# Kernel tuning notes

Hardware: AMD Instinct MI355X
Metric: run time of the kernel (lower is better)

## Reference

```python
import jax, jax.numpy as jnp
import numpy as np

B, LTEXT, LVIS, D, H = 16, 128, 4096, 1024, 16
HD = D // H


def setup_inputs() -> dict:
    key = jax.random.key(0)
    ks = jax.random.split(key, 8)
    s = 0.02
    return {
        'hidden_states': jax.random.normal(ks[0], (B, LVIS, D), jnp.float32),
        'text_states': jax.random.normal(ks[1], (LTEXT, B, D), jnp.float32),
        'Wq': jax.random.normal(ks[2], (D, D), jnp.float32) * s,
        'bq': jnp.zeros((D,), jnp.float32),
        'Wk': jax.random.normal(ks[3], (D, D), jnp.float32) * s,
        'bk': jnp.zeros((D,), jnp.float32),
        'Wv': jax.random.normal(ks[4], (D, D), jnp.float32) * s,
        'bv': jnp.zeros((D,), jnp.float32),
        'Wo': jax.random.normal(ks[5], (D, D), jnp.float32) * s,
        'bo': jnp.zeros((D,), jnp.float32),
    }


def reference(hidden_states, text_states, Wq, bq, Wk, bk, Wv, bv, Wo, bo):
    # text_states: (L_text, B, D) -- code unpacks text_len, bsz from dims 0,1
    # hidden_states: (B, L_vis, D) -- key/value source
    Ltext, bsz, d = text_states.shape
    Lvis = hidden_states.shape[1]
    scale = HD ** -0.5

    # projections (torch Linear x @ W.T + b, here W stored already transposed)
    q = (text_states @ Wq + bq) * scale
    # faithful to torch .view: flatten memory then reshape to (B, Ltext, H, hd)
    q = q.reshape(bsz, Ltext, H, HD).transpose(0, 2, 1, 3)        # (B,H,Lt,hd)
    k = (hidden_states @ Wk + bk).reshape(bsz, Lvis, H, HD).transpose(0, 2, 1, 3)
    v = (hidden_states @ Wv + bv).reshape(bsz, Lvis, H, HD).transpose(0, 2, 1, 3)

    attn = jax.nn.softmax(jnp.einsum('bhtd,bhsd->bhts', q, k), axis=-1)  # (B,H,Lt,Lv)
    text_guided_vision = jnp.einsum('bhts,bhsd->bhtd', attn, v)          # (B,H,Lt,hd)
    # second matmul with transposed attention weights: P^T @ (P V)
    out = jnp.einsum('bhts,bhtd->bhsd', attn, text_guided_vision)        # (B,H,Lv,hd)

    out = out.transpose(0, 2, 1, 3).reshape(bsz, Lvis, d)
    return out @ Wo + bo
```

## Files before the change

### kernel.cpp

```cpp
#include <hip/hip_runtime.h>
#include <stdint.h>

typedef short  s16x8 __attribute__((ext_vector_type(8)));
typedef float  f32x4 __attribute__((ext_vector_type(4)));

__device__ __forceinline__ unsigned short f2bf(float f) {
  unsigned u = __builtin_bit_cast(unsigned, f);
  u = (u + 0x7fffu + ((u >> 16) & 1u)) >> 16;
  return (unsigned short)u;
}

__device__ __forceinline__ void glds16(const void* g, void* l) {
  __builtin_amdgcn_global_load_lds((const __attribute__((address_space(1))) void*)g,
                                   (__attribute__((address_space(3))) void*)l, 16, 0, 0);
}

__device__ __forceinline__ f32x4 mfma16(s16x8 a, s16x8 b, f32x4 c) {
  return __builtin_amdgcn_mfma_f32_16x16x32_bf16(a, b, c, 0, 0, 0);
}

__global__ __launch_bounds__(256) void kt_cvt(const float* __restrict__ X,
                                              unsigned short* __restrict__ Y) {
  const size_t N8 = (size_t)16 * 4096 * 1024 / 8;
  for (size_t i = (size_t)blockIdx.x * 256 + threadIdx.x; i < N8;
       i += (size_t)gridDim.x * 256) {
    const float* g = X + i * 8;
    f32x4 a = *(const f32x4*)g;
    f32x4 b = *(const f32x4*)(g + 4);
    s16x8 o;
    o[0]=f2bf(a[0]); o[1]=f2bf(a[1]); o[2]=f2bf(a[2]); o[3]=f2bf(a[3]);
    o[4]=f2bf(b[0]); o[5]=f2bf(b[1]); o[6]=f2bf(b[2]); o[7]=f2bf(b[3]);
    *(s16x8*)(Y + i * 8) = o;
  }
}

__global__ void kt_transpose(const float* __restrict__ W, unsigned short* __restrict__ WT) {
  __shared__ float tile[64][65];
  int n0 = blockIdx.x * 64, k0 = blockIdx.y * 64;
  int tx = threadIdx.x, ty = threadIdx.y;
  #pragma unroll
  for (int r = ty; r < 64; r += 4)
    tile[r][tx] = W[(size_t)(k0 + r) * 1024 + n0 + tx];
  __syncthreads();
  #pragma unroll
  for (int r = ty; r < 64; r += 4)
    WT[(size_t)(n0 + r) * 1024 + k0 + tx] = f2bf(tile[tx][r]);
}

template <int MODE>
__global__ __launch_bounds__(256, 2) void kt_gemm(
    const void* __restrict__ Ain, const unsigned short* __restrict__ BT,
    const float* __restrict__ bias, void* __restrict__ Cout) {
  __shared__ __align__(16) unsigned short As[128 * 32];
  __shared__ __align__(16) unsigned short Bs[128 * 32];
  const int tid = threadIdx.x, lane = tid & 63, wave = tid >> 6;
  const int l15 = lane & 15, quad = lane >> 4;
  const int wr = wave >> 1, wc = wave & 1;
  const int n0 = blockIdx.x * 128, m0 = blockIdx.y * 128;

  f32x4 acc[4][4] = {};
  for (int k0 = 0; k0 < 1024; k0 += 32) {
    __syncthreads();
    #pragma unroll
    for (int i = 0; i < 2; ++i) {
      int rowb = (wave * 2 + i) * 16 + (lane >> 2);
      glds16(BT + (size_t)(n0 + rowb) * 1024 + k0 + (lane & 3) * 8,
             &Bs[(wave * 2 + i) * 512]);
    }
    if constexpr (MODE == 1) {
      const unsigned short* A = (const unsigned short*)Ain;
      #pragma unroll
      for (int i = 0; i < 2; ++i) {
        int rowa = (wave * 2 + i) * 16 + (lane >> 2);
        glds16(A + (size_t)(m0 + rowa) * 1024 + k0 + (lane & 3) * 8,
               &As[(wave * 2 + i) * 512]);
      }
    } else {
      const float* A = (const float*)Ain;
      int row = tid >> 1, ks = (tid & 1) * 16;
      const float* g = &A[(size_t)(m0 + row) * 1024 + k0 + ks];
      f32x4 fa = *(const f32x4*)(g);
      f32x4 fb = *(const f32x4*)(g + 4);
      f32x4 fc = *(const f32x4*)(g + 8);
      f32x4 fd = *(const f32x4*)(g + 12);
      s16x8 lo, hi;
      lo[0]=f2bf(fa[0]); lo[1]=f2bf(fa[1]); lo[2]=f2bf(fa[2]); lo[3]=f2bf(fa[3]);
      lo[4]=f2bf(fb[0]); lo[5]=f2bf(fb[1]); lo[6]=f2bf(fb[2]); lo[7]=f2bf(fb[3]);
      hi[0]=f2bf(fc[0]); hi[1]=f2bf(fc[1]); hi[2]=f2bf(fc[2]); hi[3]=f2bf(fc[3]);
      hi[4]=f2bf(fd[0]); hi[5]=f2bf(fd[1]); hi[6]=f2bf(fd[2]); hi[7]=f2bf(fd[3]);
      *(s16x8*)&As[row * 32 + ks] = lo;
      *(s16x8*)&As[row * 32 + ks + 8] = hi;
    }
    __syncthreads();
    s16x8 a[4], b[4];
    #pragma unroll
    for (int i = 0; i < 4; ++i) a[i] = *(const s16x8*)&As[(wr * 64 + i * 16 + l15) * 32 + quad * 8];
    #pragma unroll
    for (int j = 0; j < 4; ++j) b[j] = *(const s16x8*)&Bs[(wc * 64 + j * 16 + l15) * 32 + quad * 8];
    #pragma unroll
    for (int i = 0; i < 4; ++i)
      #pragma unroll
      for (int j = 0; j < 4; ++j) acc[i][j] = mfma16(a[i], b[j], acc[i][j]);
  }
  #pragma unroll
  for (int j = 0; j < 4; ++j) {
    int col = n0 + wc * 64 + j * 16 + l15;
    float bv = bias[col];
    #pragma unroll
    for (int i = 0; i < 4; ++i)
      #pragma unroll
      for (int r = 0; r < 4; ++r) {
        int row = m0 + wr * 64 + i * 16 + quad * 4 + r;
        float v = acc[i][j][r] + bv;
        if constexpr (MODE == 0) {
          v *= 0.125f;
          size_t idx = ((size_t)((row >> 7) * 16 + (col >> 6)) * 128 + (row & 127)) * 64 + (col & 63);
          ((unsigned short*)Cout)[idx] = f2bf(v);
        } else {
          ((float*)Cout)[(size_t)row * 1024 + col] = v;
        }
      }
  }
}

__global__ __launch_bounds__(256, 2) void kt_gemm_kv(
    const unsigned short* __restrict__ A, const unsigned short* __restrict__ BTk,
    const unsigned short* __restrict__ BTv, const float* __restrict__ biask,
    const float* __restrict__ biasv, unsigned short* __restrict__ Ko,
    unsigned short* __restrict__ Vo) {
  __shared__ __align__(16) unsigned short As[128 * 32];
  __shared__ __align__(16) unsigned short BsK[128 * 32];
  __shared__ __align__(16) unsigned short BsV[128 * 32];
  const int tid = threadIdx.x, lane = tid & 63, wave = tid >> 6;
  const int l15 = lane & 15, quad = lane >> 4;
  const int wr = wave >> 1, wc = wave & 1;
  const int n0 = blockIdx.x * 128, m0 = blockIdx.y * 128;
  f32x4 accK[4][4] = {}, accV[4][4] = {};
  for (int k0 = 0; k0 < 1024; k0 += 32) {
    __syncthreads();
    #pragma unroll
    for (int i = 0; i < 2; ++i) {
      int rowt = (wave * 2 + i) * 16 + (lane >> 2);
      int colo = (lane & 3) * 8;
      size_t goffb = (size_t)(n0 + rowt) * 1024 + k0 + colo;
      glds16(BTk + goffb, &BsK[(wave * 2 + i) * 512]);
      glds16(BTv + goffb, &BsV[(wave * 2 + i) * 512]);
      glds16(A + (size_t)(m0 + rowt) * 1024 + k0 + colo, &As[(wave * 2 + i) * 512]);
    }
    __syncthreads();
    s16x8 a[4], bk_[4], bv_[4];
    #pragma unroll
    for (int i = 0; i < 4; ++i) a[i] = *(const s16x8*)&As[(wr * 64 + i * 16 + l15) * 32 + quad * 8];
    #pragma unroll
    for (int j = 0; j < 4; ++j) bk_[j] = *(const s16x8*)&BsK[(wc * 64 + j * 16 + l15) * 32 + quad * 8];
    #pragma unroll
    for (int j = 0; j < 4; ++j) bv_[j] = *(const s16x8*)&BsV[(wc * 64 + j * 16 + l15) * 32 + quad * 8];
    #pragma unroll
    for (int i = 0; i < 4; ++i)
      #pragma unroll
      for (int j = 0; j < 4; ++j) {
        accK[i][j] = mfma16(a[i], bk_[j], accK[i][j]);
        accV[i][j] = mfma16(a[i], bv_[j], accV[i][j]);
      }
  }
  #pragma unroll
  for (int j = 0; j < 4; ++j) {
    int col = n0 + wc * 64 + j * 16 + l15;
    float bkv = biask[col], bvv = biasv[col];
    int hcol = col >> 6, dcol = col & 63;
    #pragma unroll
    for (int i = 0; i < 4; ++i)
      #pragma unroll
      for (int r = 0; r < 4; ++r) {
        int row = m0 + wr * 64 + i * 16 + quad * 4 + r;
        int bb = row >> 12, s = row & 4095;
        Ko[(((size_t)bb * 16 + hcol) * 4096 + s) * 64 + dcol] = f2bf(accK[i][j][r] + bkv);
        Vo[(((size_t)bb * 16 + hcol) * 64 + dcol) * 4096 + s] = f2bf(accV[i][j][r] + bvv);
      }
  }
}

__global__ __launch_bounds__(256, 2) void kt_attn1(
    const unsigned short* __restrict__ Qb, const unsigned short* __restrict__ Kb,
    const unsigned short* __restrict__ Vt, float* __restrict__ RpT,
    float* __restrict__ Zp) {
  __shared__ __align__(16) unsigned short Ks[128 * 64];
  __shared__ __align__(16) unsigned short Vts[64 * 128];
  __shared__ __align__(16) unsigned short Es[128 * 128];
  const int tid = threadIdx.x, lane = tid & 63, wave = tid >> 6;
  const int l15 = lane & 15, quad = lane >> 4;
  const int qidx = blockIdx.x, h = blockIdx.y, b = blockIdx.z;
  const int bh = b * 16 + h;
  const size_t kbase = (size_t)bh * 4096 * 64;
  const size_t vbase = (size_t)bh * 64 * 4096;
  s16x8 qa[2][2];
  #pragma unroll
  for (int i = 0; i < 2; ++i)
    #pragma unroll
    for (int kk = 0; kk < 2; ++kk)
      qa[i][kk] = *(const s16x8*)&Qb[((size_t)bh * 128 + wave * 32 + i * 16 + l15) * 64 + kk * 32 + quad * 8];
  s16x8 bones;
  { unsigned short o = (l15 == 0) ? (unsigned short)0x3F80 : (unsigned short)0;
    #pragma unroll
    for (int c2 = 0; c2 < 8; ++c2) bones[c2] = (short)o; }
  f32x4 Racc[2][4] = {};
  f32x4 Zacc[2] = {};
  for (int ch = 0; ch < 8; ++ch) {
    const int s0 = qidx * 1024 + ch * 128;
    __syncthreads();
    #pragma unroll
    for (int i = 0; i < 4; ++i) {
      int srow = (wave * 4 + i) * 8 + (lane >> 3);
      glds16(Kb + kbase + (size_t)(s0 + srow) * 64 + (lane & 7) * 8, &Ks[(wave * 4 + i) * 512]);
    }
    #pragma unroll
    for (int i = 0; i < 4; ++i) {
      int drow = (wave * 4 + i) * 4 + (lane >> 4);
      glds16(Vt + vbase + (size_t)drow * 4096 + s0 + (lane & 15) * 8, &Vts[(wave * 4 + i) * 512]);
    }
    __syncthreads();
    f32x4 Sacc[2][8] = {};
    #pragma unroll
    for (int kk = 0; kk < 2; ++kk) {
      s16x8 bk_[8];
      #pragma unroll
      for (int j = 0; j < 8; ++j)
        bk_[j] = *(const s16x8*)&Ks[(j * 16 + l15) * 64 + kk * 32 + quad * 8];
      #pragma unroll
      for (int i = 0; i < 2; ++i)
        #pragma unroll
        for (int j = 0; j < 8; ++j) Sacc[i][j] = mfma16(qa[i][kk], bk_[j], Sacc[i][j]);
    }
    #pragma unroll
    for (int i = 0; i < 2; ++i)
      #pragma unroll
      for (int j = 0; j < 8; ++j)
        #pragma unroll
        for (int r = 0; r < 4; ++r)
          Es[(wave * 32 + i * 16 + quad * 4 + r) * 128 + j * 16 + l15] = f2bf(__expf(Sacc[i][j][r]));
    #pragma unroll
    for (int kk = 0; kk < 4; ++kk) {
      s16x8 ea[2];
      #pragma unroll
      for (int i2 = 0; i2 < 2; ++i2)
        ea[i2] = *(const s16x8*)&Es[(wave * 32 + i2 * 16 + l15) * 128 + kk * 32 + quad * 8];
      s16x8 bv_[4];
      #pragma unroll
      for (int jd = 0; jd < 4; ++jd)
        bv_[jd] = *(const s16x8*)&Vts[(jd * 16 + l15) * 128 + kk * 32 + quad * 8];
      #pragma unroll
      for (int i2 = 0; i2 < 2; ++i2) {
        #pragma unroll
        for (int jd = 0; jd < 4; ++jd) Racc[i2][jd] = mfma16(ea[i2], bv_[jd], Racc[i2][jd]);
        Zacc[i2] = mfma16(ea[i2], bones, Zacc[i2]);
      }
    }
  }
  #pragma unroll
  for (int i2 = 0; i2 < 2; ++i2) {
    int t0 = wave * 32 + i2 * 16 + quad * 4;
    #pragma unroll
    for (int jd = 0; jd < 4; ++jd) {
      int d = jd * 16 + l15;
      *(f32x4*)&RpT[(((size_t)qidx * 256 + bh) * 64 + d) * 128 + t0] = Racc[i2][jd];
    }
    if (l15 == 0) {
      #pragma unroll
      for (int r = 0; r < 4; ++r)
        Zp[((size_t)qidx * 256 + bh) * 128 + t0 + r] = Zacc[i2][r];
    }
  }
}

__global__ void kt_reduce(const float* __restrict__ RpT, const float* __restrict__ Zp,
                          unsigned short* __restrict__ Gt) {
  size_t id = (size_t)blockIdx.x * 256 + threadIdx.x;
  int t = (int)(id & 127);
  size_t bh = id >> 13;
  float z = 0.f, r = 0.f;
  #pragma unroll
  for (int q = 0; q < 4; ++q) {
    z += Zp[(size_t)q * 32768 + bh * 128 + t];
    r += RpT[(size_t)q * 2097152 + id];
  }
  Gt[id] = f2bf(r / (z * z));
}

__global__ __launch_bounds__(256, 2) void kt_attn2(
    const unsigned short* __restrict__ Qb, const unsigned short* __restrict__ Kb,
    const unsigned short* __restrict__ Gt, unsigned short* __restrict__ Ao) {
  __shared__ __align__(16) unsigned short Ks[64 * 64];
  __shared__ __align__(16) unsigned short EsT[64 * 136];
  const int tid = threadIdx.x, lane = tid & 63, wave = tid >> 6;
  const int l15 = lane & 15, quad = lane >> 4;
  const int c = blockIdx.x, h = blockIdx.y, b = blockIdx.z;
  const int bh = b * 16 + h;
  s16x8 qf[8][2], gf[4][4];
  #pragma unroll
  for (int jt = 0; jt < 8; ++jt)
    #pragma unroll
    for (int kk = 0; kk < 2; ++kk)
      qf[jt][kk] = *(const s16x8*)&Qb[((size_t)bh * 128 + jt * 16 + l15) * 64 + kk * 32 + quad * 8];
  #pragma unroll
  for (int jd = 0; jd < 4; ++jd)
    #pragma unroll
    for (int kk = 0; kk < 4; ++kk)
      gf[jd][kk] = *(const s16x8*)&Gt[((size_t)bh * 64 + jd * 16 + l15) * 128 + kk * 32 + quad * 8];
  const size_t kbase = (size_t)bh * 4096 * 64;
  for (int it = 0; it < 16; ++it) {
    const int s0 = c * 1024 + it * 64;
    __syncthreads();
    #pragma unroll
    for (int i = 0; i < 2; ++i) {
      int srow = (wave * 2 + i) * 8 + (lane >> 3);
      glds16(Kb + kbase + (size_t)(s0 + srow) * 64 + (lane & 7) * 8, &Ks[(wave * 2 + i) * 512]);
    }
    __syncthreads();
    f32x4 Sacc[8] = {};
    #pragma unroll
    for (int kk = 0; kk < 2; ++kk) {
      s16x8 a = *(const s16x8*)&Ks[(wave * 16 + l15) * 64 + kk * 32 + quad * 8];
      #pragma unroll
      for (int jt = 0; jt < 8; ++jt) Sacc[jt] = mfma16(a, qf[jt][kk], Sacc[jt]);
    }
    #pragma unroll
    for (int jt = 0; jt < 8; ++jt)
      #pragma unroll
      for (int r = 0; r < 4; ++r)
        EsT[(wave * 16 + quad * 4 + r) * 136 + jt * 16 + l15] = f2bf(__expf(Sacc[jt][r]));
    f32x4 Oacc[4] = {};
    #pragma unroll
    for (int kk = 0; kk < 4; ++kk) {
      s16x8 ea = *(const s16x8*)&EsT[(wave * 16 + l15) * 136 + kk * 32 + quad * 8];
      #pragma unroll
      for (int jd = 0; jd < 4; ++jd) Oacc[jd] = mfma16(ea, gf[jd][kk], Oacc[jd]);
    }
    #pragma unroll
    for (int jd = 0; jd < 4; ++jd)
      #pragma unroll
      for (int r = 0; r < 4; ++r) {
        int s = s0 + wave * 16 + quad * 4 + r;
        int d = jd * 16 + l15;
        Ao[((size_t)b * 4096 + s) * 1024 + h * 64 + d] = f2bf(Oacc[jd][r]);
      }
  }
}

extern "C" void kernel_launch(void* const* d_in, const int* in_sizes, int n_in,
                              void* d_out, int out_size, void* d_ws, size_t ws_size,
                              hipStream_t stream) {
  const float* hidden = (const float*)d_in[0];
  const float* text   = (const float*)d_in[1];
  const float* Wq = (const float*)d_in[2]; const float* bq = (const float*)d_in[3];
  const float* Wk = (const float*)d_in[4]; const float* bk = (const float*)d_in[5];
  const float* Wv = (const float*)d_in[6]; const float* bv = (const float*)d_in[7];
  const float* Wo = (const float*)d_in[8]; const float* bo = (const float*)d_in[9];
  char* ws = (char*)d_ws;
  unsigned short* WqT = (unsigned short*)(ws + (size_t)0);
  unsigned short* WkT = (unsigned short*)(ws + ((size_t)2 << 20));
  unsigned short* WvT = (unsigned short*)(ws + ((size_t)4 << 20));
  unsigned short* WoT = (unsigned short*)(ws + ((size_t)6 << 20));
  unsigned short* Qb  = (unsigned short*)(ws + ((size_t)8 << 20));
  unsigned short* Kb  = (unsigned short*)(ws + ((size_t)12 << 20));
  unsigned short* Vt  = (unsigned short*)(ws + ((size_t)140 << 20));
  unsigned short* Hb  = (unsigned short*)(ws + ((size_t)268 << 20));
  unsigned short* Ao  = (unsigned short*)(ws + ((size_t)268 << 20));
  float*          RpT = (float*)(ws + ((size_t)396 << 20));
  float*          Zp  = (float*)(ws + ((size_t)428 << 20));
  unsigned short* Gt  = (unsigned short*)(ws + ((size_t)429 << 20));

  dim3 blk(256);
  kt_transpose<<<dim3(16, 16), dim3(64, 4), 0, stream>>>(Wq, WqT);
  kt_transpose<<<dim3(16, 16), dim3(64, 4), 0, stream>>>(Wk, WkT);
  kt_transpose<<<dim3(16, 16), dim3(64, 4), 0, stream>>>(Wv, WvT);
  kt_transpose<<<dim3(16, 16), dim3(64, 4), 0, stream>>>(Wo, WoT);
  kt_cvt<<<dim3(2048), blk, 0, stream>>>(hidden, Hb);
  kt_gemm<0><<<dim3(8, 16), blk, 0, stream>>>(text, WqT, bq, Qb);
  kt_gemm_kv<<<dim3(8, 512), blk, 0, stream>>>(Hb, WkT, WvT, bk, bv, Kb, Vt);
  kt_attn1<<<dim3(4, 16, 16), blk, 0, stream>>>(Qb, Kb, Vt, RpT, Zp);
  kt_reduce<<<dim3(8192), blk, 0, stream>>>(RpT, Zp, Gt);
  kt_attn2<<<dim3(4, 16, 16), blk, 0, stream>>>(Qb, Kb, Gt, Ao);
  kt_gemm<1><<<dim3(8, 512), blk, 0, stream>>>(Ao, WoT, bo, d_out);
}
```

Baseline: 1.276 ms.

## Replace K/V and output GEMMs with pipelined 256x256-tile double-buffered GEMM kernel

```diff
diff --git a/kernel.cpp b/kernel.cpp
--- a/kernel.cpp
+++ b/kernel.cpp
@@ -3,6 +3,7 @@
 
 typedef short  s16x8 __attribute__((ext_vector_type(8)));
 typedef float  f32x4 __attribute__((ext_vector_type(4)));
+typedef unsigned short u16x4 __attribute__((ext_vector_type(4)));
 
 __device__ __forceinline__ unsigned short f2bf(float f) {
   unsigned u = __builtin_bit_cast(unsigned, f);
@@ -18,6 +19,9 @@
 __device__ __forceinline__ f32x4 mfma16(s16x8 a, s16x8 b, f32x4 c) {
   return __builtin_amdgcn_mfma_f32_16x16x32_bf16(a, b, c, 0, 0, 0);
 }
+
+#define VM4 asm volatile("s_waitcnt vmcnt(4)" ::: "memory")
+#define VM0 asm volatile("s_waitcnt vmcnt(0)" ::: "memory")
 
 __global__ __launch_bounds__(256) void kt_cvt(const float* __restrict__ X,
                                               unsigned short* __restrict__ Y) {
@@ -47,10 +51,9 @@
     WT[(size_t)(n0 + r) * 1024 + k0 + tx] = f2bf(tile[tx][r]);
 }
 
-template <int MODE>
-__global__ __launch_bounds__(256, 2) void kt_gemm(
-    const void* __restrict__ Ain, const unsigned short* __restrict__ BT,
-    const float* __restrict__ bias, void* __restrict__ Cout) {
+__global__ __launch_bounds__(256, 2) void kt_gemm_q(
+    const float* __restrict__ Ain, const unsigned short* __restrict__ BT,
+    const float* __restrict__ bias, unsigned short* __restrict__ Cout) {
   __shared__ __align__(16) unsigned short As[128 * 32];
   __shared__ __align__(16) unsigned short Bs[128 * 32];
   const int tid = threadIdx.x, lane = tid & 63, wave = tid >> 6;
@@ -67,16 +70,8 @@
       glds16(BT + (size_t)(n0 + rowb) * 1024 + k0 + (lane & 3) * 8,
              &Bs[(wave * 2 + i) * 512]);
     }
-    if constexpr (MODE == 1) {
-      const unsigned short* A = (const unsigned short*)Ain;
-      #pragma unroll
-      for (int i = 0; i < 2; ++i) {
-        int rowa = (wave * 2 + i) * 16 + (lane >> 2);
-        glds16(A + (size_t)(m0 + rowa) * 1024 + k0 + (lane & 3) * 8,
-               &As[(wave * 2 + i) * 512]);
-      }
-    } else {
-      const float* A = (const float*)Ain;
+    {
+      const float* A = Ain;
       int row = tid >> 1, ks = (tid & 1) * 16;
       const float* g = &A[(size_t)(m0 + row) * 1024 + k0 + ks];
       f32x4 fa = *(const f32x4*)(g);
@@ -111,72 +106,136 @@
       #pragma unroll
       for (int r = 0; r < 4; ++r) {
         int row = m0 + wr * 64 + i * 16 + quad * 4 + r;
-        float v = acc[i][j][r] + bv;
-        if constexpr (MODE == 0) {
-          v *= 0.125f;
-          size_t idx = ((size_t)((row >> 7) * 16 + (col >> 6)) * 128 + (row & 127)) * 64 + (col & 63);
-          ((unsigned short*)Cout)[idx] = f2bf(v);
-        } else {
-          ((float*)Cout)[(size_t)row * 1024 + col] = v;
-        }
+        float v = (acc[i][j][r] + bv) * 0.125f;
+        size_t idx = ((size_t)((row >> 7) * 16 + (col >> 6)) * 128 + (row & 127)) * 64 + (col & 63);
+        Cout[idx] = f2bf(v);
       }
   }
 }
 
-__global__ __launch_bounds__(256, 2) void kt_gemm_kv(
-    const unsigned short* __restrict__ A, const unsigned short* __restrict__ BTk,
-    const unsigned short* __restrict__ BTv, const float* __restrict__ biask,
-    const float* __restrict__ biasv, unsigned short* __restrict__ Ko,
-    unsigned short* __restrict__ Vo) {
-  __shared__ __align__(16) unsigned short As[128 * 32];
-  __shared__ __align__(16) unsigned short BsK[128 * 32];
-  __shared__ __align__(16) unsigned short BsV[128 * 32];
+template <int MODE>
+__global__ __launch_bounds__(512, 2) void kt_gemm256(
+    const unsigned short* __restrict__ A, const unsigned short* __restrict__ BT,
+    const float* __restrict__ bias, void* __restrict__ Cout) {
+  __shared__ __align__(16) unsigned short lds[65536];
   const int tid = threadIdx.x, lane = tid & 63, wave = tid >> 6;
   const int l15 = lane & 15, quad = lane >> 4;
-  const int wr = wave >> 1, wc = wave & 1;
-  const int n0 = blockIdx.x * 128, m0 = blockIdx.y * 128;
-  f32x4 accK[4][4] = {}, accV[4][4] = {};
-  for (int k0 = 0; k0 < 1024; k0 += 32) {
-    __syncthreads();
-    #pragma unroll
-    for (int i = 0; i < 2; ++i) {
-      int rowt = (wave * 2 + i) * 16 + (lane >> 2);
-      int colo = (lane & 3) * 8;
-      size_t goffb = (size_t)(n0 + rowt) * 1024 + k0 + colo;
-      glds16(BTk + goffb, &BsK[(wave * 2 + i) * 512]);
-      glds16(BTv + goffb, &BsV[(wave * 2 + i) * 512]);
-      glds16(A + (size_t)(m0 + rowt) * 1024 + k0 + colo, &As[(wave * 2 + i) * 512]);
-    }
-    __syncthreads();
-    s16x8 a[4], bk_[4], bv_[4];
-    #pragma unroll
-    for (int i = 0; i < 4; ++i) a[i] = *(const s16x8*)&As[(wr * 64 + i * 16 + l15) * 32 + quad * 8];
-    #pragma unroll
-    for (int j = 0; j < 4; ++j) bk_[j] = *(const s16x8*)&BsK[(wc * 64 + j * 16 + l15) * 32 + quad * 8];
-    #pragma unroll
-    for (int j = 0; j < 4; ++j) bv_[j] = *(const s16x8*)&BsV[(wc * 64 + j * 16 + l15) * 32 + quad * 8];
-    #pragma unroll
-    for (int i = 0; i < 4; ++i)
-      #pragma unroll
-      for (int j = 0; j < 4; ++j) {
-        accK[i][j] = mfma16(a[i], bk_[j], accK[i][j]);
-        accV[i][j] = mfma16(a[i], bv_[j], accV[i][j]);
+  const int wr = wave >> 2, wc = wave & 3;
+  const int r0 = lane >> 3, sck = (lane & 7) ^ r0;
+  const int nblk = blockIdx.x & 3, mblk = blockIdx.x >> 2;
+  const int n0 = nblk * 256, m0 = mblk * 256;
+  const unsigned short* Asrc = A + (size_t)m0 * 1024;
+  const unsigned short* Bsrc = BT + (size_t)n0 * 1024;
+
+  f32x4 acc[8][4] = {};
+  s16x8 bf_[4][2];
+
+  auto stageA = [&](int t, int h, int buf) {
+    #pragma unroll
+    for (int is = 0; is < 2; ++is) {
+      int c = wave * 2 + is;
+      glds16(Asrc + (size_t)(h * 128 + c * 8 + r0) * 1024 + t * 64 + sck * 8,
+             &lds[buf * 32768 + h * 8192 + c * 512]);
+    }
+  };
+  auto stageB = [&](int t, int h, int buf) {
+    #pragma unroll
+    for (int is = 0; is < 2; ++is) {
+      int c = wave * 2 + is;
+      glds16(Bsrc + (size_t)(h * 128 + c * 8 + r0) * 1024 + t * 64 + sck * 8,
+             &lds[buf * 32768 + 16384 + h * 8192 + c * 512]);
+    }
+  };
+
+  stageA(0, 0, 0); stageA(0, 1, 0); stageB(0, 0, 0); stageB(0, 1, 0);
+  stageB(1, 0, 1); stageB(1, 1, 1);
+  VM4;
+  __builtin_amdgcn_s_barrier();
+
+  #pragma unroll 1
+  for (int it = 0; it < 8; ++it) {
+    const bool last = (it == 7);
+    const int te = 2 * it;
+    #pragma unroll
+    for (int half = 0; half < 2; ++half) {
+      const int buf = half;
+      #pragma unroll
+      for (int p = 0; p < 4; ++p) {
+        if (p == 0) {
+          #pragma unroll
+          for (int j = 0; j < 4; ++j)
+            #pragma unroll
+            for (int kk = 0; kk < 2; ++kk) {
+              int r = (wc & 1) * 64 + j * 16 + l15;
+              bf_[j][kk] = *(const s16x8*)&lds[buf * 32768 + 16384 + (wc >> 1) * 8192
+                                               + r * 64 + (((kk * 4 + quad) ^ (r & 7)) << 3)];
+            }
+        }
+        s16x8 af[2][2];
+        #pragma unroll
+        for (int ii = 0; ii < 2; ++ii)
+          #pragma unroll
+          for (int kk = 0; kk < 2; ++kk) {
+            int r = (p * 2 + ii) * 16 + l15;
+            af[ii][kk] = *(const s16x8*)&lds[buf * 32768 + wr * 8192
+                                             + r * 64 + (((kk * 4 + quad) ^ (r & 7)) << 3)];
+          }
+        if (half == 0) {
+          if (p == 0) { stageA(te + 1, 0, 1); stageA(te + 1, 1, 1); }
+          else if (p == 1) { if (!last) stageB(te + 2, 0, 0); }
+          else if (p == 2) { if (!last) stageB(te + 2, 1, 0); }
+        } else {
+          if (p == 0) { if (!last) stageA(te + 2, 0, 0); }
+          else if (p == 1) { if (!last) { stageA(te + 2, 1, 0); stageB(te + 3, 0, 1); } }
+          else if (p == 2) { if (!last) stageB(te + 3, 1, 1); }
+        }
+        __builtin_amdgcn_s_barrier();
+        __builtin_amdgcn_s_setprio(1);
+        #pragma unroll
+        for (int ii = 0; ii < 2; ++ii)
+          #pragma unroll
+          for (int j = 0; j < 4; ++j)
+            #pragma unroll
+            for (int kk = 0; kk < 2; ++kk)
+              acc[p * 2 + ii][j] = mfma16(af[ii][kk], bf_[j][kk], acc[p * 2 + ii][j]);
+        __builtin_amdgcn_s_setprio(0);
+        if (p == 3) {
+          if (half == 0) { if (last) { VM0; } else { VM4; } }
+          else           { if (!last) { VM4; } }
+        }
+        __builtin_amdgcn_s_barrier();
       }
-  }
+    }
+  }
+
+  const int bb = m0 >> 12;
   #pragma unroll
   for (int j = 0; j < 4; ++j) {
-    int col = n0 + wc * 64 + j * 16 + l15;
-    float bkv = biask[col], bvv = biasv[col];
-    int hcol = col >> 6, dcol = col & 63;
-    #pragma unroll
-    for (int i = 0; i < 4; ++i)
-      #pragma unroll
-      for (int r = 0; r < 4; ++r) {
-        int row = m0 + wr * 64 + i * 16 + quad * 4 + r;
-        int bb = row >> 12, s = row & 4095;
-        Ko[(((size_t)bb * 16 + hcol) * 4096 + s) * 64 + dcol] = f2bf(accK[i][j][r] + bkv);
-        Vo[(((size_t)bb * 16 + hcol) * 64 + dcol) * 4096 + s] = f2bf(accV[i][j][r] + bvv);
+    const int col = n0 + wc * 64 + j * 16 + l15;
+    const float bv = bias[col];
+    const int hcol = col >> 6, dcol = col & 63;
+    #pragma unroll
+    for (int i = 0; i < 8; ++i) {
+      const int row0 = m0 + wr * 128 + i * 16 + quad * 4;
+      const int s = row0 & 4095;
+      if constexpr (MODE == 0) {
+        unsigned short* Ko = (unsigned short*)Cout;
+        size_t base = (((size_t)bb * 16 + hcol) * 4096 + s) * 64 + dcol;
+        #pragma unroll
+        for (int r = 0; r < 4; ++r) Ko[base + (size_t)r * 64] = f2bf(acc[i][j][r] + bv);
+      } else if constexpr (MODE == 1) {
+        size_t base = (((size_t)bb * 16 + hcol) * 64 + dcol) * 4096 + s;
+        u16x4 w;
+        #pragma unroll
+        for (int r = 0; r < 4; ++r) w[r] = f2bf(acc[i][j][r] + bv);
+        *(u16x4*)&((unsigned short*)Cout)[base] = w;
+      } else {
+        float* O = (float*)Cout;
+        size_t base = (size_t)row0 * 1024 + col;
+        #pragma unroll
+        for (int r = 0; r < 4; ++r) O[base + (size_t)r * 1024] = acc[i][j][r] + bv;
       }
+    }
   }
 }
 
@@ -375,10 +434,11 @@
   kt_transpose<<<dim3(16, 16), dim3(64, 4), 0, stream>>>(Wv, WvT);
   kt_transpose<<<dim3(16, 16), dim3(64, 4), 0, stream>>>(Wo, WoT);
   kt_cvt<<<dim3(2048), blk, 0, stream>>>(hidden, Hb);
-  kt_gemm<0><<<dim3(8, 16), blk, 0, stream>>>(text, WqT, bq, Qb);
-  kt_gemm_kv<<<dim3(8, 512), blk, 0, stream>>>(Hb, WkT, WvT, bk, bv, Kb, Vt);
+  kt_gemm_q<<<dim3(8, 16), blk, 0, stream>>>(text, WqT, bq, Qb);
+  kt_gemm256<0><<<dim3(1024), dim3(512), 0, stream>>>(Hb, WkT, bk, Kb);
+  kt_gemm256<1><<<dim3(1024), dim3(512), 0, stream>>>(Hb, WvT, bv, Vt);
   kt_attn1<<<dim3(4, 16, 16), blk, 0, stream>>>(Qb, Kb, Vt, RpT, Zp);
   kt_reduce<<<dim3(8192), blk, 0, stream>>>(RpT, Zp, Gt);
   kt_attn2<<<dim3(4, 16, 16), blk, 0, stream>>>(Qb, Kb, Gt, Ao);
-  kt_gemm<1><<<dim3(8, 512), blk, 0, stream>>>(Ao, WoT, bo, d_out);
-}
+  kt_gemm256<2><<<dim3(1024), dim3(512), 0, stream>>>(Ao, WoT, bo, d_out);
+}
```

After: 1.193 ms. 1.07x faster.
